# Kernel optimization log

Measured on AMD Instinct MI355X. Metric: run time of the kernel, lower is better.

Reference implementation:

```python
import jax, jax.numpy as jnp
import numpy as np

GRID = 256          # grid_size
PAD = 30            # padding_size
GLOBAL = GRID + 2 * PAD   # 316
OUT = 512           # deform_input_size
K = 2 * PAD + 1     # 61 Gaussian kernel


def make_gaussian(size=K, a=1.0, b=0.5, fwhm1=100.0, fwhm2=25.0):
    x = np.arange(size, dtype=np.float64)
    c = size // 2
    r2 = (x[None, :] - c) ** 2 + (x[:, None] - c) ** 2
    g1 = np.exp(-4.0 * np.log(2.0) * r2 / fwhm1 ** 2)
    g2 = np.exp(-4.0 * np.log(2.0) * r2 / fwhm2 ** 2)
    return (a * g1 - b * g2).astype(np.float32)


def p_basis():
    # P[0,i,j] = (j - PAD)/(GRID-1) ; P[1,i,j] = (i - PAD)/(GRID-1)
    coord = (jnp.arange(GLOBAL, dtype=jnp.float32) - PAD) / (GRID - 1.0)
    px = jnp.broadcast_to(coord[None, :], (GLOBAL, GLOBAL))
    py = jnp.broadcast_to(coord[:, None], (GLOBAL, GLOBAL))
    return jnp.stack([px, py], axis=0)  # [2, 316, 316]


def base_grid():
    lin = jnp.linspace(-1.0, 1.0, OUT, dtype=jnp.float32)
    w = jnp.broadcast_to(lin[None, :], (OUT, OUT))  # x varies along columns
    h = jnp.broadcast_to(lin[:, None], (OUT, OUT))  # y varies along rows
    return jnp.stack([w, h], axis=-1)  # [512, 512, 2]


def grid_sample_bilinear(img, grid):
    """F.grid_sample, mode=bilinear, padding_mode=zeros, align_corners=True.
    img: [B,C,H,W], grid: [B,Hg,Wg,2] with (x,y) in [-1,1]."""
    B, C, H, W = img.shape
    gx = (grid[..., 0] + 1.0) * (W - 1) * 0.5
    gy = (grid[..., 1] + 1.0) * (H - 1) * 0.5
    x0 = jnp.floor(gx); y0 = jnp.floor(gy)
    wx1 = gx - x0; wx0 = 1.0 - wx1
    wy1 = gy - y0; wy0 = 1.0 - wy1

    def gather(ix, iy):
        valid = ((ix >= 0) & (ix <= W - 1) & (iy >= 0) & (iy <= H - 1)).astype(img.dtype)
        ixc = jnp.clip(ix, 0, W - 1).astype(jnp.int32)
        iyc = jnp.clip(iy, 0, H - 1).astype(jnp.int32)
        v = jax.vmap(lambda im, yy, xx: im[:, yy, xx])(img, iyc, ixc)  # [B,C,Hg,Wg]
        return v * valid[:, None]

    out = (gather(x0, y0) * (wx0 * wy0)[:, None]
           + gather(x0 + 1, y0) * (wx1 * wy0)[:, None]
           + gather(x0, y0 + 1) * (wx0 * wy1)[:, None]
           + gather(x0 + 1, y0 + 1) * (wx1 * wy1)[:, None])
    return out


def setup_inputs() -> dict:
    key = jax.random.key(0)
    k1, k2 = jax.random.split(key)
    x = jax.random.normal(k1, (8, 32, 512, 512), dtype=jnp.float32)
    xs = jax.random.uniform(k2, (8, 1, 256, 256), dtype=jnp.float32)
    gauss_kernel = jnp.asarray(make_gaussian())  # [61,61] fixed conv weight
    return {"x": x, "xs": xs, "gauss_kernel": gauss_kernel}


def reference(x, xs, gauss_kernel):
    B = xs.shape[0]
    xs = xs.reshape(B, 1, GRID, GRID)
    # ReplicationPad2d(PAD)
    xs_hm = jnp.pad(xs, ((0, 0), (0, 0), (PAD, PAD), (PAD, PAD)), mode="edge")  # [B,1,316,316]
    P = p_basis()  # [2,316,316]
    # channel 0: xs_hm (-> p_filter); channels 1,2: P * xs (-> x/y numerators)
    stacked = jnp.concatenate([xs_hm, P[None] * xs_hm], axis=1)  # [B,3,316,316]
    inp = stacked.reshape(B * 3, 1, GLOBAL, GLOBAL)
    kern = gauss_kernel.reshape(1, 1, K, K)
    conv = jax.lax.conv_general_dilated(inp, kern, (1, 1), "VALID")  # [B*3,1,256,256]
    conv = conv.reshape(B, 3, GRID, GRID)
    p_f = conv[:, 0]
    x_f = conv[:, 1] / p_f
    y_f = conv[:, 2] / p_f
    xg = jnp.clip(x_f * 2.0 - 1.0, -1.0, 1.0)
    yg = jnp.clip(y_f * 2.0 - 1.0, -1.0, 1.0)
    grid = jnp.stack([xg, yg], axis=1)  # [B,2,256,256]
    # nn.Upsample bilinear (align_corners=False) == jax.image.resize half-pixel bilinear
    grid_up = jax.image.resize(grid, (B, 2, OUT, OUT), method="bilinear")
    grid_l = jnp.transpose(grid_up, (0, 2, 3, 1))  # [B,512,512,2]
    grid_r = (49.0 * base_grid()[None] + grid_l) / 50.0
    x_sampled = grid_sample_bilinear(x, grid_r)  # [B,C,512,512]
    return x_sampled, grid_up
```

## Files before the change

kernel.cpp:

```cpp
#include <hip/hip_runtime.h>
#include <math.h>

#define GRID_N 256
#define PADN   30
#define GLOB_N 316
#define KS     61
#define OUT_N  512
#define BATCH  8
#define CHAN   32

#define TW     128
#define TH     8
#define SROWS  13
#define SCOLS  144
#define SC4    36
#define NSLOT  (SROWS * SC4)

typedef float v4f __attribute__((ext_vector_type(4)));

__device__ __forceinline__ void compute_weights(float* w1, float* w2) {
    int t = threadIdx.x;
    if (t < KS) {
        double d  = (double)(t - PADN);
        double r2 = d * d;
        const double c = 2.772588722239781;
        w1[t] = (float)exp(-c * r2 / 10000.0);
        w2[t] = (float)exp(-c * r2 / 625.0);
    }
}

__global__ __launch_bounds__(256) void hpass_kernel(const float* __restrict__ xs,
                                                    float* __restrict__ H) {
    __shared__ float srow[GLOB_N];
    __shared__ float w1[KS], w2[KS];
    int b  = blockIdx.x / GLOB_N;
    int gi = blockIdx.x % GLOB_N;
    int t  = threadIdx.x;

    compute_weights(w1, w2);

    int iy = gi - PADN;
    iy = iy < 0 ? 0 : (iy > GRID_N - 1 ? GRID_N - 1 : iy);
    const float* src = xs + ((size_t)b * GRID_N + iy) * GRID_N;
    for (int j = t; j < GLOB_N; j += 256) {
        int ix = j - PADN;
        ix = ix < 0 ? 0 : (ix > GRID_N - 1 ? GRID_N - 1 : ix);
        srow[j] = src[ix];
    }
    __syncthreads();

    float a1 = 0.f, a2 = 0.f, a3 = 0.f, a4 = 0.f;
    for (int v = 0; v < KS; ++v) {
        float s  = srow[t + v];
        float cc = (float)(t + v - PADN) * (1.0f / 255.0f);
        float cs = cc * s;
        float cw1 = w1[v], cw2 = w2[v];
        a1 += cw1 * s;
        a2 += cw2 * s;
        a3 += cw1 * cs;
        a4 += cw2 * cs;
    }
    size_t cst  = (size_t)GLOB_N * GRID_N;
    size_t base = ((size_t)(b * 4) * GLOB_N + gi) * GRID_N + t;
    H[base]           = a1;
    H[base + cst]     = a2;
    H[base + 2 * cst] = a3;
    H[base + 3 * cst] = a4;
}

__global__ __launch_bounds__(256) void vpass_kernel(const float* __restrict__ H,
                                                    float* __restrict__ g256) {
    __shared__ float w1[KS], w2[KS];
    int bid = (int)blockIdx.x;
    bid = (bid & 7) * 256 + (bid >> 3);
    int b = bid >> 8;
    int y = bid & 255;
    int t = threadIdx.x;

    compute_weights(w1, w2);
    __syncthreads();

    const float* Hb = H + (size_t)b * 4 * GLOB_N * GRID_N;
    size_t cst = (size_t)GLOB_N * GRID_N;

    float s1 = 0.f, s2 = 0.f, sx1 = 0.f, sx2 = 0.f, sy1 = 0.f, sy2 = 0.f;
    for (int u = 0; u < KS; ++u) {
        size_t off = (size_t)(y + u) * GRID_N + t;
        float h1 = Hb[off];
        float h2 = Hb[off + cst];
        float h3 = Hb[off + 2 * cst];
        float h4 = Hb[off + 3 * cst];
        float cw1 = w1[u], cw2 = w2[u];
        float cc = (float)(y + u - PADN) * (1.0f / 255.0f);
        s1  += cw1 * h1;
        s2  += cw2 * h2;
        sx1 += cw1 * h3;
        sx2 += cw2 * h4;
        sy1 += cw1 * (cc * h1);
        sy2 += cw2 * (cc * h2);
    }
    float p  = s1 - 0.5f * s2;
    float xf = (sx1 - 0.5f * sx2) / p;
    float yf = (sy1 - 0.5f * sy2) / p;
    float xg = fminf(fmaxf(xf * 2.0f - 1.0f, -1.0f), 1.0f);
    float yg = fminf(fmaxf(yf * 2.0f - 1.0f, -1.0f), 1.0f);

    size_t o = (size_t)(b * 2) * GRID_N * GRID_N + (size_t)y * GRID_N + t;
    g256[o] = xg;
    g256[o + (size_t)GRID_N * GRID_N] = yg;
}

__global__ __launch_bounds__(256) void upsample_kernel(const float* __restrict__ g256,
                                                       float* __restrict__ gup) {
    int idx = blockIdx.x * 256 + threadIdx.x;
    int ox = idx & (OUT_N - 1);
    int oy = (idx >> 9) & (OUT_N - 1);
    int b  = idx >> 18;

    float sx = 0.5f * (float)ox - 0.25f;
    float sy = 0.5f * (float)oy - 0.25f;
    float fxf = floorf(sx), fyf = floorf(sy);
    int x0 = (int)fxf, y0 = (int)fyf;
    float fx = sx - fxf, fy = sy - fyf;
    int x0c = x0 < 0 ? 0 : x0;
    int x1c = x0 + 1 > GRID_N - 1 ? GRID_N - 1 : x0 + 1;
    int y0c = y0 < 0 ? 0 : y0;
    int y1c = y0 + 1 > GRID_N - 1 ? GRID_N - 1 : y0 + 1;

    for (int c = 0; c < 2; ++c) {
        const float* g = g256 + ((size_t)(b * 2 + c)) * GRID_N * GRID_N;
        float v00 = g[y0c * GRID_N + x0c];
        float v10 = g[y0c * GRID_N + x1c];
        float v01 = g[y1c * GRID_N + x0c];
        float v11 = g[y1c * GRID_N + x1c];
        float v = (v00 * (1.f - fx) + v10 * fx) * (1.f - fy)
                + (v01 * (1.f - fx) + v11 * fx) * fy;
        gup[((size_t)(b * 2 + c)) * OUT_N * OUT_N + (size_t)oy * OUT_N + ox] = v;
    }
}

__global__ __launch_bounds__(256) void sample_kernel(const float* __restrict__ x,
                                                     const float* __restrict__ gup,
                                                     float* __restrict__ out) {
    __shared__ float tile[SROWS * SCOLS];

    int bid = (int)blockIdx.x;
    bid = (bid & 7) * 256 + (bid >> 3);
    int b  = bid >> 8;
    int tb = bid & 255;
    int tx = (tb & 3) * TW;
    int ty = (tb >> 2) * TH;

    int t   = threadIdx.x;
    int col = t & (TW - 1);
    int kk  = t >> 7;

    int row_base = ty - 2;
    int col_base = tx - 8;

    int off0 = 0, off1 = 0;
    {
        int k = t;
        int r = k / SC4, i = k - r * SC4;
        int rg = row_base + r; rg = rg < 0 ? 0 : (rg > OUT_N - 1 ? OUT_N - 1 : rg);
        int cg = col_base + i * 4; cg = cg < 0 ? 0 : (cg > OUT_N - 4 ? OUT_N - 4 : cg);
        off0 = rg * OUT_N + cg;
        k = t + 256;
        if (k < NSLOT) {
            r = k / SC4; i = k - r * SC4;
            rg = row_base + r; rg = rg < 0 ? 0 : (rg > OUT_N - 1 ? OUT_N - 1 : rg);
            cg = col_base + i * 4; cg = cg < 0 ? 0 : (cg > OUT_N - 4 ? OUT_N - 4 : cg);
            off1 = rg * OUT_N + cg;
        }
    }
    bool has1 = (t + 256) < NSLOT;

    float w00[4], w10[4], w01[4], w11[4];
    int lbase[4];
    {
        size_t gplane = (size_t)OUT_N * OUT_N;
        int ox = tx + col;
        float bx = -1.0f + (float)ox * (2.0f / 511.0f);
        #pragma unroll
        for (int j = 0; j < 4; ++j) {
            int oy = ty + kk + 2 * j;
            size_t gidx = (size_t)(b * 2) * gplane + (size_t)oy * OUT_N + ox;
            float gxu = gup[gidx];
            float gyu = gup[gidx + gplane];
            float by = -1.0f + (float)oy * (2.0f / 511.0f);
            float gx = (49.0f * bx + gxu) * 0.02f;
            float gy = (49.0f * by + gyu) * 0.02f;
            float pxf = (gx + 1.0f) * 255.5f;
            float pyf = (gy + 1.0f) * 255.5f;
            float fx0 = floorf(pxf), fy0 = floorf(pyf);
            int x0 = (int)fx0, y0 = (int)fy0;
            float fx = pxf - fx0, fy = pyf - fy0;
            w00[j] = (1.f - fx) * (1.f - fy);
            w10[j] = fx * (1.f - fy);
            w01[j] = (1.f - fx) * fy;
            w11[j] = fx * fy;
            lbase[j] = (y0 - row_base) * SCOLS + (x0 - col_base);
        }
    }

    size_t plane = (size_t)OUT_N * OUT_N;
    const float* xb = x + (size_t)b * CHAN * plane;
    float* ob = out + (size_t)b * CHAN * plane;
    int ocol = tx + col;

    v4f pf0 = *(const v4f*)(xb + off0);
    v4f pf1 = has1 ? *(const v4f*)(xb + off1) : pf0;

    for (int c = 0; c < CHAN; ++c) {
        __syncthreads();
        *(v4f*)(tile + t * 4) = pf0;
        if (has1) *(v4f*)(tile + (t + 256) * 4) = pf1;
        __syncthreads();

        if (c + 1 < CHAN) {
            const float* xc = xb + (size_t)(c + 1) * plane;
            pf0 = *(const v4f*)(xc + off0);
            if (has1) pf1 = *(const v4f*)(xc + off1);
        }

        float* oc = ob + (size_t)c * plane;
        #pragma unroll
        for (int j = 0; j < 4; ++j) {
            int lb = lbase[j];
            float v00 = tile[lb];
            float v10 = tile[lb + 1];
            float v01 = tile[lb + SCOLS];
            float v11 = tile[lb + SCOLS + 1];
            float v = w00[j] * v00 + w10[j] * v10 + w01[j] * v01 + w11[j] * v11;
            int oy = ty + kk + 2 * j;
            __builtin_nontemporal_store(v, oc + (size_t)oy * OUT_N + ocol);
        }
    }
}

extern "C" void kernel_launch(void* const* d_in, const int* in_sizes, int n_in,
                              void* d_out, int out_size, void* d_ws, size_t ws_size,
                              hipStream_t stream) {
    (void)in_sizes; (void)n_in; (void)d_ws; (void)ws_size; (void)out_size;
    const float* x  = (const float*)d_in[0];
    const float* xs = (const float*)d_in[1];

    float* out = (float*)d_out;
    const size_t XS_OUT = (size_t)BATCH * CHAN * OUT_N * OUT_N;
    float* gup = out + XS_OUT;

    float* H    = out;
    float* g256 = out + 4u * 1024 * 1024;

    hipLaunchKernelGGL(hpass_kernel, dim3(BATCH * GLOB_N), dim3(256), 0, stream, xs, H);
    hipLaunchKernelGGL(vpass_kernel, dim3(BATCH * GRID_N), dim3(256), 0, stream, H, g256);
    hipLaunchKernelGGL(upsample_kernel, dim3(BATCH * OUT_N * OUT_N / 256), dim3(256), 0, stream,
                       g256, gup);
    hipLaunchKernelGGL(sample_kernel, dim3(BATCH * OUT_N * OUT_N / (TW * TH)), dim3(256), 0, stream,
                       x, gup, out);
}
```

Baseline: 154.6 us.

## Fuse grid upsample into sample kernel and double-buffer channel tiles

The bilinear upsample of the 256x256 deformation grid now happens inside the sampling kernel. Each tile computes the upsampled grid values it needs from g256, which is placed in workspace, and writes the grid_up output directly. This removes a separate launch and a write-then-read round trip of the upsampled grid. The channel loop also moves to a two-buffer shared tile with a two-channel-deep register prefetch, which cuts one barrier's worth of load latency per channel at the cost of more LDS and registers. The fused path runs only when the workspace is large enough to hold g256; otherwise the old path is kept.

```diff
diff --git a/kernel.cpp b/kernel.cpp
--- a/kernel.cpp
+++ b/kernel.cpp
@@ -15,6 +15,7 @@
 #define SCOLS  144
 #define SC4    36
 #define NSLOT  (SROWS * SC4)
+#define TSZ    (SROWS * SCOLS)
 
 typedef float v4f __attribute__((ext_vector_type(4)));
 
@@ -139,10 +140,13 @@
     }
 }
 
+template <int FUSED>
 __global__ __launch_bounds__(256) void sample_kernel(const float* __restrict__ x,
-                                                     const float* __restrict__ gup,
+                                                     const float* __restrict__ g256,
+                                                     const float* __restrict__ gup_in,
+                                                     float* __restrict__ gup_out,
                                                      float* __restrict__ out) {
-    __shared__ float tile[SROWS * SCOLS];
+    __shared__ float tile[2 * TSZ];
 
     int bid = (int)blockIdx.x;
     bid = (bid & 7) * 256 + (bid >> 3);
@@ -178,15 +182,55 @@
     float w00[4], w10[4], w01[4], w11[4];
     int lbase[4];
     {
-        size_t gplane = (size_t)OUT_N * OUT_N;
         int ox = tx + col;
         float bx = -1.0f + (float)ox * (2.0f / 511.0f);
+
+        float usx = 0.5f * (float)ox - 0.25f;
+        float ufxf = floorf(usx);
+        int ux0 = (int)ufxf;
+        float ufx = usx - ufxf;
+        int ux0c = ux0 < 0 ? 0 : ux0;
+        int ux1c = ux0 + 1 > GRID_N - 1 ? GRID_N - 1 : ux0 + 1;
+        const float* g0 = g256 + (size_t)(b * 2) * GRID_N * GRID_N;
+        const float* g1 = g0 + GRID_N * GRID_N;
+        size_t gplane = (size_t)OUT_N * OUT_N;
+
         #pragma unroll
         for (int j = 0; j < 4; ++j) {
             int oy = ty + kk + 2 * j;
-            size_t gidx = (size_t)(b * 2) * gplane + (size_t)oy * OUT_N + ox;
-            float gxu = gup[gidx];
-            float gyu = gup[gidx + gplane];
+            float gxu, gyu;
+            if (FUSED) {
+                float usy = 0.5f * (float)oy - 0.25f;
+                float ufyf = floorf(usy);
+                int uy0 = (int)ufyf;
+                float ufy = usy - ufyf;
+                int uy0c = uy0 < 0 ? 0 : uy0;
+                int uy1c = uy0 + 1 > GRID_N - 1 ? GRID_N - 1 : uy0 + 1;
+                {
+                    float v00 = g0[uy0c * GRID_N + ux0c];
+                    float v10 = g0[uy0c * GRID_N + ux1c];
+                    float v01 = g0[uy1c * GRID_N + ux0c];
+                    float v11 = g0[uy1c * GRID_N + ux1c];
+                    gxu = (v00 * (1.f - ufx) + v10 * ufx) * (1.f - ufy)
+                        + (v01 * (1.f - ufx) + v11 * ufx) * ufy;
+                }
+                {
+                    float v00 = g1[uy0c * GRID_N + ux0c];
+                    float v10 = g1[uy0c * GRID_N + ux1c];
+                    float v01 = g1[uy1c * GRID_N + ux0c];
+                    float v11 = g1[uy1c * GRID_N + ux1c];
+                    gyu = (v00 * (1.f - ufx) + v10 * ufx) * (1.f - ufy)
+                        + (v01 * (1.f - ufx) + v11 * ufx) * ufy;
+                }
+                size_t gidx = (size_t)(b * 2) * gplane + (size_t)oy * OUT_N + ox;
+                __builtin_nontemporal_store(gxu, gup_out + gidx);
+                __builtin_nontemporal_store(gyu, gup_out + gidx + gplane);
+            } else {
+                size_t gidx = (size_t)(b * 2) * gplane + (size_t)oy * OUT_N + ox;
+                gxu = gup_in[gidx];
+                gyu = gup_in[gidx + gplane];
+            }
+
             float by = -1.0f + (float)oy * (2.0f / 511.0f);
             float gx = (49.0f * bx + gxu) * 0.02f;
             float gy = (49.0f * by + gyu) * 0.02f;
@@ -208,29 +252,32 @@
     float* ob = out + (size_t)b * CHAN * plane;
     int ocol = tx + col;
 
-    v4f pf0 = *(const v4f*)(xb + off0);
-    v4f pf1 = has1 ? *(const v4f*)(xb + off1) : pf0;
+    v4f pfA0 = *(const v4f*)(xb + off0);
+    v4f pfA1 = has1 ? *(const v4f*)(xb + off1) : pfA0;
+    v4f pfB0 = *(const v4f*)(xb + plane + off0);
+    v4f pfB1 = has1 ? *(const v4f*)(xb + plane + off1) : pfB0;
 
     for (int c = 0; c < CHAN; ++c) {
+        float* tb_ = tile + (c & 1) * TSZ;
         __syncthreads();
-        *(v4f*)(tile + t * 4) = pf0;
-        if (has1) *(v4f*)(tile + (t + 256) * 4) = pf1;
+        *(v4f*)(tb_ + t * 4) = pfA0;
+        if (has1) *(v4f*)(tb_ + (t + 256) * 4) = pfA1;
+        pfA0 = pfB0; pfA1 = pfB1;
+        if (c + 2 < CHAN) {
+            const float* xc = xb + (size_t)(c + 2) * plane;
+            pfB0 = *(const v4f*)(xc + off0);
+            if (has1) pfB1 = *(const v4f*)(xc + off1);
+        }
         __syncthreads();
-
-        if (c + 1 < CHAN) {
-            const float* xc = xb + (size_t)(c + 1) * plane;
-            pf0 = *(const v4f*)(xc + off0);
-            if (has1) pf1 = *(const v4f*)(xc + off1);
-        }
 
         float* oc = ob + (size_t)c * plane;
         #pragma unroll
         for (int j = 0; j < 4; ++j) {
             int lb = lbase[j];
-            float v00 = tile[lb];
-            float v10 = tile[lb + 1];
-            float v01 = tile[lb + SCOLS];
-            float v11 = tile[lb + SCOLS + 1];
+            float v00 = tb_[lb];
+            float v10 = tb_[lb + 1];
+            float v01 = tb_[lb + SCOLS];
+            float v11 = tb_[lb + SCOLS + 1];
             float v = w00[j] * v00 + w10[j] * v10 + w01[j] * v01 + w11[j] * v11;
             int oy = ty + kk + 2 * j;
             __builtin_nontemporal_store(v, oc + (size_t)oy * OUT_N + ocol);
@@ -241,7 +288,7 @@
 extern "C" void kernel_launch(void* const* d_in, const int* in_sizes, int n_in,
                               void* d_out, int out_size, void* d_ws, size_t ws_size,
                               hipStream_t stream) {
-    (void)in_sizes; (void)n_in; (void)d_ws; (void)ws_size; (void)out_size;
+    (void)in_sizes; (void)n_in; (void)out_size;
     const float* x  = (const float*)d_in[0];
     const float* xs = (const float*)d_in[1];
 
@@ -249,13 +296,20 @@
     const size_t XS_OUT = (size_t)BATCH * CHAN * OUT_N * OUT_N;
     float* gup = out + XS_OUT;
 
-    float* H    = out;
-    float* g256 = out + 4u * 1024 * 1024;
+    float* H = out;
+    const size_t G256_BYTES = (size_t)BATCH * 2 * GRID_N * GRID_N * sizeof(float);
+    bool fused = ws_size >= G256_BYTES;
+    float* g256 = fused ? (float*)d_ws : out + 4u * 1024 * 1024;
 
     hipLaunchKernelGGL(hpass_kernel, dim3(BATCH * GLOB_N), dim3(256), 0, stream, xs, H);
     hipLaunchKernelGGL(vpass_kernel, dim3(BATCH * GRID_N), dim3(256), 0, stream, H, g256);
-    hipLaunchKernelGGL(upsample_kernel, dim3(BATCH * OUT_N * OUT_N / 256), dim3(256), 0, stream,
-                       g256, gup);
-    hipLaunchKernelGGL(sample_kernel, dim3(BATCH * OUT_N * OUT_N / (TW * TH)), dim3(256), 0, stream,
-                       x, gup, out);
-}
+    if (fused) {
+        hipLaunchKernelGGL((sample_kernel<1>), dim3(BATCH * OUT_N * OUT_N / (TW * TH)),
+                           dim3(256), 0, stream, x, g256, gup, gup, out);
+    } else {
+        hipLaunchKernelGGL(upsample_kernel, dim3(BATCH * OUT_N * OUT_N / 256), dim3(256), 0,
+                           stream, g256, gup);
+        hipLaunchKernelGGL((sample_kernel<0>), dim3(BATCH * OUT_N * OUT_N / (TW * TH)),
+                           dim3(256), 0, stream, x, g256, gup, gup, out);
+    }
+}
```

New measurement: 149.0 us. 1.04x faster.
